# Kernel optimization log

Hardware: AMD Instinct MI355X
Metric: run time of the kernel (lower is better)

## Reference

```python
import jax, jax.numpy as jnp
import numpy as np

N_LAYERS = 3
N_NODES = 100000
N_EDGES = 1600000
D = 32


def setup_inputs() -> dict:
    key = jax.random.key(0)
    k1, k2, k3, k4 = jax.random.split(key, 4)
    edge_row = jax.random.randint(k1, (N_EDGES,), 0, N_NODES, dtype=jnp.int64 if jax.config.jax_enable_x64 else jnp.int32)
    edge_col = jax.random.randint(k2, (N_EDGES,), 0, N_NODES, dtype=edge_row.dtype)
    edge_val = jax.random.uniform(k3, (N_EDGES,), dtype=jnp.float32)
    x = jax.random.normal(k4, (N_NODES, D), dtype=jnp.float32)
    return {"edge_row": edge_row, "edge_col": edge_col, "edge_val": edge_val, "x": x}


def _spmm(edge_row, edge_col, edge_val, h):
    # y[r] = sum_{edges e with row r} val[e] * h[col[e]]  -- COO SpMM
    msgs = edge_val[:, None] * h[edge_col]  # [E, D]
    return jax.ops.segment_sum(msgs, edge_row, num_segments=N_NODES)


def reference(edge_row, edge_col, edge_val, x):
    # LightGCN propagation: mean over layer-0..n_layers embeddings
    out = x
    acc = x
    for _ in range(N_LAYERS):
        out = _spmm(edge_row, edge_col, edge_val, out)
        acc = acc + out
    return acc / jnp.asarray(N_LAYERS + 1, dtype=x.dtype)
```

## Files before the change

kernel.cpp:

```cpp
#include <hip/hip_runtime.h>


#define NN 100000
#define NE 1600000
#define DD 32
#define CHUNK 4096
#define NCHUNK ((NE + CHUNK - 1) / CHUNK)
#define BROWS 128
#define NBKT ((NN + BROWS - 1) / BROWS)
#define LDSE 3072

__device__ __forceinline__ unsigned f2bf(float f) {
    unsigned u = __float_as_uint(f);
    return (u + 0x7fffu + ((u >> 16) & 1u)) >> 16;
}

typedef float    fv4 __attribute__((ext_vector_type(4)));
typedef int      iv2 __attribute__((ext_vector_type(2)));
typedef unsigned uv4 __attribute__((ext_vector_type(4)));

__device__ __forceinline__ int2 ldnt_e(const int2* p) {
    iv2 v = __builtin_nontemporal_load((const iv2*)p);
    return make_int2(v.x, v.y);
}
__device__ __forceinline__ float4 ldnt_f4(const float4* p) {
    fv4 v = __builtin_nontemporal_load((const fv4*)p);
    return make_float4(v.x, v.y, v.z, v.w);
}
__device__ __forceinline__ void stnt_f4(float4* p, float4 f) {
    fv4 v = {f.x, f.y, f.z, f.w};
    __builtin_nontemporal_store(v, (fv4*)p);
}
__device__ __forceinline__ void stnt_u4(uint4* p, uint4 f) {
    uv4 v = {f.x, f.y, f.z, f.w};
    __builtin_nontemporal_store(v, (uv4*)p);
}


__global__ __launch_bounds__(1024) void hist_kernel(
    const int* __restrict__ row, int* __restrict__ H)
{
    __shared__ int cnt[NBKT];
    const int tid = threadIdx.x;
    const int start = blockIdx.x * CHUNK;
    const int n = min(CHUNK, NE - start);
    for (int k = tid; k < NBKT; k += 1024) cnt[k] = 0;
    __syncthreads();
    const int j = tid * 4;
    if (j + 3 < n) {
        int4 r4 = *(const int4*)(row + start + j);
        atomicAdd(&cnt[r4.x >> 7], 1);
        atomicAdd(&cnt[r4.y >> 7], 1);
        atomicAdd(&cnt[r4.z >> 7], 1);
        atomicAdd(&cnt[r4.w >> 7], 1);
    } else {
        for (int k = j; k < n; k++) atomicAdd(&cnt[row[start + k] >> 7], 1);
    }
    __syncthreads();
    int* Hrow = H + (size_t)blockIdx.x * NBKT;
    for (int k = tid; k < NBKT; k += 1024) Hrow[k] = cnt[k];
}


__global__ __launch_bounds__(1024) void scan_tr_kernel(
    const int* __restrict__ H, int* __restrict__ Pt, int* __restrict__ tot)
{
    const int b = blockIdx.x * 16 + (threadIdx.x >> 6);
    if (b >= NBKT) return;
    const int lane = threadIdx.x & 63;
    int run = 0;
    #pragma unroll
    for (int c0 = 0; c0 < NCHUNK; c0 += 64) {
        int c = c0 + lane;
        int v = (c < NCHUNK) ? H[(size_t)c * NBKT + b] : 0;
        int x = v;
        #pragma unroll
        for (int off = 1; off < 64; off <<= 1) {
            int y = __shfl_up(x, off, 64);
            if (lane >= off) x += y;
        }
        if (c < NCHUNK) Pt[(size_t)b * NCHUNK + c] = run + x - v;
        run += __shfl(x, 63, 64);
    }
    if (lane == 0) tot[b] = run;
}


__global__ __launch_bounds__(1024) void scan_buckets_kernel(
    const int* __restrict__ tot, int* __restrict__ bucketbase,
    int* __restrict__ row_ptr)
{
    const int tid = threadIdx.x;
    int v = (tid < NBKT) ? tot[tid] : 0;
    int lane = tid & 63, w = tid >> 6;
    int x = v;
    #pragma unroll
    for (int off = 1; off < 64; off <<= 1) {
        int y = __shfl_up(x, off, 64);
        if (lane >= off) x += y;
    }
    __shared__ int wt[16];
    if (lane == 63) wt[w] = x;
    __syncthreads();
    if (w == 0 && lane < 16) {
        int y = wt[lane];
        #pragma unroll
        for (int off = 1; off < 16; off <<= 1) {
            int z = __shfl_up(y, off, 16);
            if ((lane & 15) >= off) y += z;
        }
        wt[lane] = y;
    }
    __syncthreads();
    int wo = (w > 0) ? wt[w - 1] : 0;
    int excl = x + wo - v;
    if (tid < NBKT) bucketbase[tid] = excl;
    if (tid == NBKT) { bucketbase[NBKT] = NE; row_ptr[NN] = NE; }
}


__global__ __launch_bounds__(1024) void scatter_kernel(
    const int* __restrict__ row, const int* __restrict__ col,
    const float* __restrict__ val, const int* __restrict__ bucketbase,
    const int* __restrict__ Pt, int2* __restrict__ tmp)
{
    __shared__ int cnt[NBKT];
    __shared__ int lbase[NBKT];
    __shared__ int gofs[NBKT];
    __shared__ int wt[16];
    __shared__ int2 recs[CHUNK];
    __shared__ int dest[CHUNK];
    const int tid = threadIdx.x;
    const int start = blockIdx.x * CHUNK;
    const int n = min(CHUNK, NE - start);
    for (int k = tid; k < NBKT; k += 1024) cnt[k] = 0;
    __syncthreads();

    int rrow[CHUNK / 1024], rcol[CHUNK / 1024], rank[CHUNK / 1024];
    float rval[CHUNK / 1024];
    #pragma unroll
    for (int k = 0; k < CHUNK / 1024; k++) {
        int j = k * 1024 + tid;
        if (j < n) {
            int r = row[start + j];
            rrow[k] = r;
            rcol[k] = col[start + j];
            rval[k] = val[start + j];
            rank[k] = atomicAdd(&cnt[r >> 7], 1);
        } else {
            rrow[k] = -1;
        }
    }
    __syncthreads();

    int v = (tid < NBKT) ? cnt[tid] : 0;
    {
        int lane = tid & 63, w = tid >> 6;
        int x = v;
        #pragma unroll
        for (int off = 1; off < 64; off <<= 1) {
            int y = __shfl_up(x, off, 64);
            if (lane >= off) x += y;
        }
        if (lane == 63) wt[w] = x;
        __syncthreads();
        if (w == 0 && lane < 16) {
            int y = wt[lane];
            #pragma unroll
            for (int off = 1; off < 16; off <<= 1) {
                int z = __shfl_up(y, off, 16);
                if ((lane & 15) >= off) y += z;
            }
            wt[lane] = y;
        }
        __syncthreads();
        int excl = x + ((w > 0) ? wt[w - 1] : 0) - v;
        if (tid < NBKT) {
            lbase[tid] = excl;
            gofs[tid] = bucketbase[tid] + Pt[(size_t)tid * NCHUNK + blockIdx.x];
        }
    }
    __syncthreads();

    #pragma unroll
    for (int k = 0; k < CHUNK / 1024; k++) {
        if (rrow[k] >= 0) {
            int b = rrow[k] >> 7;
            int p = lbase[b] + rank[k];
            recs[p] = make_int2(((rrow[k] & 127) << 17) | rcol[k],
                                __float_as_int(rval[k]));
            dest[p] = gofs[b] + rank[k];
        }
    }
    __syncthreads();

    for (int p = tid; p < n; p += 1024)
        tmp[dest[p]] = recs[p];
}


__global__ __launch_bounds__(512) void bucket_sort_kernel(
    const int* __restrict__ bucketbase, const int2* __restrict__ tmp,
    int* __restrict__ row_ptr, int2* __restrict__ edges)
{
    __shared__ int cntw[8][BROWS];
    __shared__ int curw[8][BROWS];
    __shared__ int wt2[2];
    __shared__ int2 ed[LDSE];
    const int tid = threadIdx.x;
    const int w   = tid >> 6;
    const int b   = blockIdx.x;
    const int s   = bucketbase[b];
    const int e   = bucketbase[b + 1];
    const int tot = e - s;

    for (int k = tid; k < 8 * BROWS; k += 512) (&cntw[0][0])[k] = 0;
    __syncthreads();

    int2 rc[6];
    #pragma unroll
    for (int k = 0; k < 6; k++) {
        int j = s + k * 512 + tid;
        rc[k] = (j < e && j < s + LDSE) ? tmp[j] : make_int2(-1, 0);
        if (rc[k].x >= 0) atomicAdd(&cntw[w][rc[k].x >> 17], 1);
    }
    if (tot > LDSE)
        for (int j = s + LDSE + tid; j < e; j += 512)
            atomicAdd(&cntw[w][tmp[j].x >> 17], 1);
    __syncthreads();

    int v = 0, x = 0;
    if (tid < BROWS) {
        int d = 0;
        #pragma unroll
        for (int ww = 0; ww < 8; ww++) d += cntw[ww][tid];
        v = d;
        int lane = tid & 63;
        x = v;
        #pragma unroll
        for (int off = 1; off < 64; off <<= 1) {
            int y = __shfl_up(x, off, 64);
            if (lane >= off) x += y;
        }
        if (lane == 63) wt2[tid >> 6] = x;
    }
    __syncthreads();
    if (tid < BROWS) {
        int excl = x + ((tid >> 6) ? wt2[0] : 0) - v;
        int r = b * BROWS + tid;
        if (r < NN) row_ptr[r] = s + excl;
        int run = excl;
        #pragma unroll
        for (int ww = 0; ww < 8; ww++) { curw[ww][tid] = run; run += cntw[ww][tid]; }
    }
    __syncthreads();

    if (tot <= LDSE) {
        #pragma unroll
        for (int k = 0; k < 6; k++) {
            if (rc[k].x >= 0) {
                int pos = atomicAdd(&curw[w][rc[k].x >> 17], 1);
                ed[pos] = make_int2(rc[k].x & 0x1FFFF, rc[k].y);
            }
        }
        __syncthreads();
        for (int k = tid; k < tot; k += 512)
            edges[s + k] = ed[k];
    } else {
        #pragma unroll
        for (int k = 0; k < 6; k++) {
            if (rc[k].x >= 0) {
                int pos = atomicAdd(&curw[w][rc[k].x >> 17], 1);
                edges[s + pos] = make_int2(rc[k].x & 0x1FFFF, rc[k].y);
            }
        }
        for (int j = s + LDSE + tid; j < e; j += 512) {
            int2 rec = tmp[j];
            int pos = atomicAdd(&curw[w][rec.x >> 17], 1);
            edges[s + pos] = make_int2(rec.x & 0x1FFFF, rec.y);
        }
    }
}


__global__ __launch_bounds__(256) void cvt_kernel(
    const float2* __restrict__ xin2, unsigned* __restrict__ hb)
{
    int j = blockIdx.x * 256 + threadIdx.x;
    if (j >= NN * DD / 2) return;
    float2 f = xin2[j];
    hb[j] = f2bf(f.x) | (f2bf(f.y) << 16);
}


template <int MODE>
__global__ __launch_bounds__(256) void spmm_kernel(
    const int* __restrict__ row_ptr, const int2* __restrict__ edges,
    const uint4* __restrict__ hb4,
    uint4* __restrict__ houtb4,
    const float4* __restrict__ xin4, float4* __restrict__ out4)
{
    const int g = blockIdx.x * 64 + (threadIdx.x >> 2);
    if (g >= NN) return;
    const int t = threadIdx.x & 3;
    const int s = row_ptr[g];
    const int e = row_ptr[g + 1];

    float acc[8] = {0.f, 0.f, 0.f, 0.f, 0.f, 0.f, 0.f, 0.f};

#define ACC8(W, V)                                                         \
    do {                                                                   \
        acc[0] += (V) * __uint_as_float((W).x << 16);                      \
        acc[1] += (V) * __uint_as_float((W).x & 0xffff0000u);              \
        acc[2] += (V) * __uint_as_float((W).y << 16);                      \
        acc[3] += (V) * __uint_as_float((W).y & 0xffff0000u);              \
        acc[4] += (V) * __uint_as_float((W).z << 16);                      \
        acc[5] += (V) * __uint_as_float((W).z & 0xffff0000u);              \
        acc[6] += (V) * __uint_as_float((W).w << 16);                      \
        acc[7] += (V) * __uint_as_float((W).w & 0xffff0000u);              \
    } while (0)

    int i = s;
    for (; i + 8 <= e; i += 8) {
        int2 a0 = ldnt_e(edges + i);
        int2 a1 = ldnt_e(edges + i + 1);
        int2 a2 = ldnt_e(edges + i + 2);
        int2 a3 = ldnt_e(edges + i + 3);
        int2 a4 = ldnt_e(edges + i + 4);
        int2 a5 = ldnt_e(edges + i + 5);
        int2 a6 = ldnt_e(edges + i + 6);
        int2 a7 = ldnt_e(edges + i + 7);
        uint4 w0 = hb4[a0.x * 4 + t];
        uint4 w1 = hb4[a1.x * 4 + t];
        uint4 w2 = hb4[a2.x * 4 + t];
        uint4 w3 = hb4[a3.x * 4 + t];
        uint4 w4 = hb4[a4.x * 4 + t];
        uint4 w5 = hb4[a5.x * 4 + t];
        uint4 w6 = hb4[a6.x * 4 + t];
        uint4 w7 = hb4[a7.x * 4 + t];
        ACC8(w0, __int_as_float(a0.y)); ACC8(w1, __int_as_float(a1.y));
        ACC8(w2, __int_as_float(a2.y)); ACC8(w3, __int_as_float(a3.y));
        ACC8(w4, __int_as_float(a4.y)); ACC8(w5, __int_as_float(a5.y));
        ACC8(w6, __int_as_float(a6.y)); ACC8(w7, __int_as_float(a7.y));
    }
    for (; i + 4 <= e; i += 4) {
        int2 a0 = ldnt_e(edges + i);
        int2 a1 = ldnt_e(edges + i + 1);
        int2 a2 = ldnt_e(edges + i + 2);
        int2 a3 = ldnt_e(edges + i + 3);
        uint4 w0 = hb4[a0.x * 4 + t];
        uint4 w1 = hb4[a1.x * 4 + t];
        uint4 w2 = hb4[a2.x * 4 + t];
        uint4 w3 = hb4[a3.x * 4 + t];
        ACC8(w0, __int_as_float(a0.y)); ACC8(w1, __int_as_float(a1.y));
        ACC8(w2, __int_as_float(a2.y)); ACC8(w3, __int_as_float(a3.y));
    }
    for (; i < e; ++i) {
        int2 a0 = ldnt_e(edges + i);
        uint4 w0 = hb4[a0.x * 4 + t];
        ACC8(w0, __int_as_float(a0.y));
    }
#undef ACC8

    if (MODE == 0 || MODE == 1) {
        uint4 p;
        p.x = f2bf(acc[0]) | (f2bf(acc[1]) << 16);
        p.y = f2bf(acc[2]) | (f2bf(acc[3]) << 16);
        p.z = f2bf(acc[4]) | (f2bf(acc[5]) << 16);
        p.w = f2bf(acc[6]) | (f2bf(acc[7]) << 16);
        stnt_u4(houtb4 + g * 4 + t, p);
    }
    const int o = g * 8 + t * 2;
    float4 lo, hi;
    if (MODE == 0) {
        float4 x0 = ldnt_f4(xin4 + o), x1 = ldnt_f4(xin4 + o + 1);
        lo = make_float4(x0.x + acc[0], x0.y + acc[1], x0.z + acc[2], x0.w + acc[3]);
        hi = make_float4(x1.x + acc[4], x1.y + acc[5], x1.z + acc[6], x1.w + acc[7]);
    } else if (MODE == 1) {
        float4 o0 = ldnt_f4(out4 + o), o1 = ldnt_f4(out4 + o + 1);
        lo = make_float4(o0.x + acc[0], o0.y + acc[1], o0.z + acc[2], o0.w + acc[3]);
        hi = make_float4(o1.x + acc[4], o1.y + acc[5], o1.z + acc[6], o1.w + acc[7]);
    } else {
        float4 o0 = ldnt_f4(out4 + o), o1 = ldnt_f4(out4 + o + 1);
        lo = make_float4((o0.x + acc[0]) * 0.25f, (o0.y + acc[1]) * 0.25f,
                         (o0.z + acc[2]) * 0.25f, (o0.w + acc[3]) * 0.25f);
        hi = make_float4((o1.x + acc[4]) * 0.25f, (o1.y + acc[5]) * 0.25f,
                         (o1.z + acc[6]) * 0.25f, (o1.w + acc[7]) * 0.25f);
    }
    stnt_f4(out4 + o, lo);
    stnt_f4(out4 + o + 1, hi);
}


extern "C" void kernel_launch(void* const* d_in, const int* in_sizes, int n_in,
                              void* d_out, int out_size, void* d_ws, size_t ws_size,
                              hipStream_t stream) {
    const int*   edge_row = (const int*)d_in[0];
    const int*   edge_col = (const int*)d_in[1];
    const float* edge_val = (const float*)d_in[2];
    const float* x        = (const float*)d_in[3];
    float* out = (float*)d_out;

    char* ws = (char*)d_ws;
    int*  H          = (int*)ws;   ws += (((size_t)NCHUNK * NBKT * 4) + 511) & ~511ull;
    int*  Pt         = (int*)ws;   ws += (((size_t)NBKT * NCHUNK * 4) + 511) & ~511ull;
    int*  tot        = (int*)ws;   ws += 4096;
    int*  bucketbase = (int*)ws;   ws += 4096;
    int*  row_ptr    = (int*)ws;   ws += ((size_t)(NN + 1) * 4 + 511) & ~511ull;
    int2* tmp        = (int2*)ws;  ws += (size_t)NE * 8 + 64;
    int2* edges      = (int2*)ws;  ws += (size_t)NE * 8 + 64;
    unsigned* hb0    = (unsigned*)ws;  ws += (size_t)NN * DD * 2;
    unsigned* hb1    = (unsigned*)ws;  ws += (size_t)NN * DD * 2;

    hist_kernel        <<<NCHUNK, 1024, 0, stream>>>(edge_row, H);
    scan_tr_kernel     <<<(NBKT + 15) / 16, 1024, 0, stream>>>(H, Pt, tot);
    scan_buckets_kernel<<<1, 1024, 0, stream>>>(tot, bucketbase, row_ptr);
    scatter_kernel     <<<NCHUNK, 1024, 0, stream>>>(edge_row, edge_col, edge_val,
                                                     bucketbase, Pt, tmp);
    bucket_sort_kernel <<<NBKT, 512, 0, stream>>>(bucketbase, tmp, row_ptr, edges);
    cvt_kernel         <<<(NN * DD / 2 + 255) / 256, 256, 0, stream>>>(
                         (const float2*)x, hb0);

    dim3 sp_grid((NN + 63) / 64);
    spmm_kernel<0><<<sp_grid, 256, 0, stream>>>(row_ptr, edges,
        (const uint4*)hb0, (uint4*)hb1, (const float4*)x, (float4*)out);
    spmm_kernel<1><<<sp_grid, 256, 0, stream>>>(row_ptr, edges,
        (const uint4*)hb1, (uint4*)hb0, (const float4*)x, (float4*)out);
    spmm_kernel<2><<<sp_grid, 256, 0, stream>>>(row_ptr, edges,
        (const uint4*)hb0, (uint4*)hb1, (const float4*)x, (float4*)out);
}
```

Before: 208.7 us.

## Fuse bf16 conversion into bucket sort and software-pipeline edge loads in SpMM

Folds the x-to-bf16 conversion into the bucket sort kernel, so each block converts 2048 float2 pairs and one kernel launch disappears. In the SpMM kernel, the next batch of 8 edge records is prefetched while the current batch's gathers are in flight, and the residual/accumulator input is loaded up front to overlap with the gather loop. Nontemporal load and store hints are dropped in favour of plain accesses. This adds register pressure from the double-buffered edge records, and the cache behaviour changes because the hints are gone.

```diff
diff --git a/kernel.cpp b/kernel.cpp
--- a/kernel.cpp
+++ b/kernel.cpp
@@ -13,27 +13,6 @@
 __device__ __forceinline__ unsigned f2bf(float f) {
     unsigned u = __float_as_uint(f);
     return (u + 0x7fffu + ((u >> 16) & 1u)) >> 16;
-}
-
-typedef float    fv4 __attribute__((ext_vector_type(4)));
-typedef int      iv2 __attribute__((ext_vector_type(2)));
-typedef unsigned uv4 __attribute__((ext_vector_type(4)));
-
-__device__ __forceinline__ int2 ldnt_e(const int2* p) {
-    iv2 v = __builtin_nontemporal_load((const iv2*)p);
-    return make_int2(v.x, v.y);
-}
-__device__ __forceinline__ float4 ldnt_f4(const float4* p) {
-    fv4 v = __builtin_nontemporal_load((const fv4*)p);
-    return make_float4(v.x, v.y, v.z, v.w);
-}
-__device__ __forceinline__ void stnt_f4(float4* p, float4 f) {
-    fv4 v = {f.x, f.y, f.z, f.w};
-    __builtin_nontemporal_store(v, (fv4*)p);
-}
-__device__ __forceinline__ void stnt_u4(uint4* p, uint4 f) {
-    uv4 v = {f.x, f.y, f.z, f.w};
-    __builtin_nontemporal_store(v, (uv4*)p);
 }
 
 
@@ -201,7 +180,8 @@
 
 __global__ __launch_bounds__(512) void bucket_sort_kernel(
     const int* __restrict__ bucketbase, const int2* __restrict__ tmp,
-    int* __restrict__ row_ptr, int2* __restrict__ edges)
+    int* __restrict__ row_ptr, int2* __restrict__ edges,
+    const float2* __restrict__ xin2, unsigned* __restrict__ hb0)
 {
     __shared__ int cntw[8][BROWS];
     __shared__ int curw[8][BROWS];
@@ -214,6 +194,15 @@
     const int e   = bucketbase[b + 1];
     const int tot = e - s;
 
+    #pragma unroll
+    for (int k = 0; k < 4; k++) {
+        int j = b * 2048 + k * 512 + tid;
+        if (j < NN * 16) {
+            float2 f = xin2[j];
+            hb0[j] = f2bf(f.x) | (f2bf(f.y) << 16);
+        }
+    }
+
     for (int k = tid; k < 8 * BROWS; k += 512) (&cntw[0][0])[k] = 0;
     __syncthreads();
 
@@ -280,16 +269,6 @@
             edges[s + pos] = make_int2(rec.x & 0x1FFFF, rec.y);
         }
     }
-}
-
-
-__global__ __launch_bounds__(256) void cvt_kernel(
-    const float2* __restrict__ xin2, unsigned* __restrict__ hb)
-{
-    int j = blockIdx.x * 256 + threadIdx.x;
-    if (j >= NN * DD / 2) return;
-    float2 f = xin2[j];
-    hb[j] = f2bf(f.x) | (f2bf(f.y) << 16);
 }
 
 
@@ -305,6 +284,11 @@
     const int t = threadIdx.x & 3;
     const int s = row_ptr[g];
     const int e = row_ptr[g + 1];
+    const int o = g * 8 + t * 2;
+
+    float4 p0, p1;
+    if (MODE == 0) { p0 = xin4[o]; p1 = xin4[o + 1]; }
+    else           { p0 = out4[o]; p1 = out4[o + 1]; }
 
     float acc[8] = {0.f, 0.f, 0.f, 0.f, 0.f, 0.f, 0.f, 0.f};
 
@@ -320,16 +304,35 @@
         acc[7] += (V) * __uint_as_float((W).w & 0xffff0000u);              \
     } while (0)
 
+    int2 a0, a1, a2, a3, a4, a5, a6, a7;
     int i = s;
-    for (; i + 8 <= e; i += 8) {
-        int2 a0 = ldnt_e(edges + i);
-        int2 a1 = ldnt_e(edges + i + 1);
-        int2 a2 = ldnt_e(edges + i + 2);
-        int2 a3 = ldnt_e(edges + i + 3);
-        int2 a4 = ldnt_e(edges + i + 4);
-        int2 a5 = ldnt_e(edges + i + 5);
-        int2 a6 = ldnt_e(edges + i + 6);
-        int2 a7 = ldnt_e(edges + i + 7);
+    if (i + 8 <= e) {
+        a0 = edges[i];     a1 = edges[i + 1];
+        a2 = edges[i + 2]; a3 = edges[i + 3];
+        a4 = edges[i + 4]; a5 = edges[i + 5];
+        a6 = edges[i + 6]; a7 = edges[i + 7];
+    }
+    for (; i + 16 <= e; i += 8) {
+        uint4 w0 = hb4[a0.x * 4 + t];
+        uint4 w1 = hb4[a1.x * 4 + t];
+        uint4 w2 = hb4[a2.x * 4 + t];
+        uint4 w3 = hb4[a3.x * 4 + t];
+        uint4 w4 = hb4[a4.x * 4 + t];
+        uint4 w5 = hb4[a5.x * 4 + t];
+        uint4 w6 = hb4[a6.x * 4 + t];
+        uint4 w7 = hb4[a7.x * 4 + t];
+        int2 b0 = edges[i + 8];  int2 b1 = edges[i + 9];
+        int2 b2 = edges[i + 10]; int2 b3 = edges[i + 11];
+        int2 b4 = edges[i + 12]; int2 b5 = edges[i + 13];
+        int2 b6 = edges[i + 14]; int2 b7 = edges[i + 15];
+        ACC8(w0, __int_as_float(a0.y)); ACC8(w1, __int_as_float(a1.y));
+        ACC8(w2, __int_as_float(a2.y)); ACC8(w3, __int_as_float(a3.y));
+        ACC8(w4, __int_as_float(a4.y)); ACC8(w5, __int_as_float(a5.y));
+        ACC8(w6, __int_as_float(a6.y)); ACC8(w7, __int_as_float(a7.y));
+        a0 = b0; a1 = b1; a2 = b2; a3 = b3;
+        a4 = b4; a5 = b5; a6 = b6; a7 = b7;
+    }
+    if (i + 8 <= e) {
         uint4 w0 = hb4[a0.x * 4 + t];
         uint4 w1 = hb4[a1.x * 4 + t];
         uint4 w2 = hb4[a2.x * 4 + t];
@@ -342,23 +345,24 @@
         ACC8(w2, __int_as_float(a2.y)); ACC8(w3, __int_as_float(a3.y));
         ACC8(w4, __int_as_float(a4.y)); ACC8(w5, __int_as_float(a5.y));
         ACC8(w6, __int_as_float(a6.y)); ACC8(w7, __int_as_float(a7.y));
+        i += 8;
     }
     for (; i + 4 <= e; i += 4) {
-        int2 a0 = ldnt_e(edges + i);
-        int2 a1 = ldnt_e(edges + i + 1);
-        int2 a2 = ldnt_e(edges + i + 2);
-        int2 a3 = ldnt_e(edges + i + 3);
-        uint4 w0 = hb4[a0.x * 4 + t];
-        uint4 w1 = hb4[a1.x * 4 + t];
-        uint4 w2 = hb4[a2.x * 4 + t];
-        uint4 w3 = hb4[a3.x * 4 + t];
-        ACC8(w0, __int_as_float(a0.y)); ACC8(w1, __int_as_float(a1.y));
-        ACC8(w2, __int_as_float(a2.y)); ACC8(w3, __int_as_float(a3.y));
+        int2 c0 = edges[i];
+        int2 c1 = edges[i + 1];
+        int2 c2 = edges[i + 2];
+        int2 c3 = edges[i + 3];
+        uint4 w0 = hb4[c0.x * 4 + t];
+        uint4 w1 = hb4[c1.x * 4 + t];
+        uint4 w2 = hb4[c2.x * 4 + t];
+        uint4 w3 = hb4[c3.x * 4 + t];
+        ACC8(w0, __int_as_float(c0.y)); ACC8(w1, __int_as_float(c1.y));
+        ACC8(w2, __int_as_float(c2.y)); ACC8(w3, __int_as_float(c3.y));
     }
     for (; i < e; ++i) {
-        int2 a0 = ldnt_e(edges + i);
-        uint4 w0 = hb4[a0.x * 4 + t];
-        ACC8(w0, __int_as_float(a0.y));
+        int2 c0 = edges[i];
+        uint4 w0 = hb4[c0.x * 4 + t];
+        ACC8(w0, __int_as_float(c0.y));
     }
 #undef ACC8
 
@@ -368,27 +372,20 @@
         p.y = f2bf(acc[2]) | (f2bf(acc[3]) << 16);
         p.z = f2bf(acc[4]) | (f2bf(acc[5]) << 16);
         p.w = f2bf(acc[6]) | (f2bf(acc[7]) << 16);
-        stnt_u4(houtb4 + g * 4 + t, p);
-    }
-    const int o = g * 8 + t * 2;
+        houtb4[g * 4 + t] = p;
+    }
     float4 lo, hi;
-    if (MODE == 0) {
-        float4 x0 = ldnt_f4(xin4 + o), x1 = ldnt_f4(xin4 + o + 1);
-        lo = make_float4(x0.x + acc[0], x0.y + acc[1], x0.z + acc[2], x0.w + acc[3]);
-        hi = make_float4(x1.x + acc[4], x1.y + acc[5], x1.z + acc[6], x1.w + acc[7]);
-    } else if (MODE == 1) {
-        float4 o0 = ldnt_f4(out4 + o), o1 = ldnt_f4(out4 + o + 1);
-        lo = make_float4(o0.x + acc[0], o0.y + acc[1], o0.z + acc[2], o0.w + acc[3]);
-        hi = make_float4(o1.x + acc[4], o1.y + acc[5], o1.z + acc[6], o1.w + acc[7]);
+    if (MODE == 0 || MODE == 1) {
+        lo = make_float4(p0.x + acc[0], p0.y + acc[1], p0.z + acc[2], p0.w + acc[3]);
+        hi = make_float4(p1.x + acc[4], p1.y + acc[5], p1.z + acc[6], p1.w + acc[7]);
     } else {
-        float4 o0 = ldnt_f4(out4 + o), o1 = ldnt_f4(out4 + o + 1);
-        lo = make_float4((o0.x + acc[0]) * 0.25f, (o0.y + acc[1]) * 0.25f,
-                         (o0.z + acc[2]) * 0.25f, (o0.w + acc[3]) * 0.25f);
-        hi = make_float4((o1.x + acc[4]) * 0.25f, (o1.y + acc[5]) * 0.25f,
-                         (o1.z + acc[6]) * 0.25f, (o1.w + acc[7]) * 0.25f);
-    }
-    stnt_f4(out4 + o, lo);
-    stnt_f4(out4 + o + 1, hi);
+        lo = make_float4((p0.x + acc[0]) * 0.25f, (p0.y + acc[1]) * 0.25f,
+                         (p0.z + acc[2]) * 0.25f, (p0.w + acc[3]) * 0.25f);
+        hi = make_float4((p1.x + acc[4]) * 0.25f, (p1.y + acc[5]) * 0.25f,
+                         (p1.z + acc[6]) * 0.25f, (p1.w + acc[7]) * 0.25f);
+    }
+    out4[o] = lo;
+    out4[o + 1] = hi;
 }
 
 
@@ -417,9 +414,8 @@
     scan_buckets_kernel<<<1, 1024, 0, stream>>>(tot, bucketbase, row_ptr);
     scatter_kernel     <<<NCHUNK, 1024, 0, stream>>>(edge_row, edge_col, edge_val,
                                                      bucketbase, Pt, tmp);
-    bucket_sort_kernel <<<NBKT, 512, 0, stream>>>(bucketbase, tmp, row_ptr, edges);
-    cvt_kernel         <<<(NN * DD / 2 + 255) / 256, 256, 0, stream>>>(
-                         (const float2*)x, hb0);
+    bucket_sort_kernel <<<NBKT, 512, 0, stream>>>(bucketbase, tmp, row_ptr, edges,
+                                                  (const float2*)x, hb0);
 
     dim3 sp_grid((NN + 63) / 64);
     spmm_kernel<0><<<sp_grid, 256, 0, stream>>>(row_ptr, edges,
```

Result: faster. 186.9 us (-10.4%).
